# Kernel tuning notes

Measured on AMD Instinct MI355X. Metric: run time of the kernel, lower is better.

Reference implementation:

```python
import jax, jax.numpy as jnp
import numpy as np

TEMP = 0.5  # init temperature
EPS = 1e-12  # F.normalize eps


def setup_inputs() -> dict:
    key = jax.random.key(0)
    k1, k2 = jax.random.split(key)
    batch_embedding = jax.random.normal(k1, (4096, 256), dtype=jnp.float32)
    labels = jax.random.randint(k2, (4096,), 0, 512, dtype=jnp.int64)
    return {"batch_embedding": batch_embedding, "labels": labels}


def reference(batch_embedding, labels):
    n = labels.shape[0]
    dt = batch_embedding.dtype
    # row-normalize; cosine_similarity of normalized rows == norm @ norm.T
    nrm = jnp.linalg.norm(batch_embedding, axis=1, keepdims=True)
    norm = batch_embedding / jnp.maximum(nrm, EPS)
    sim = norm @ norm.T  # [n, n]
    mask = (labels[:, None] == labels[None, :]).astype(dt)  # same-label pairs (incl. diagonal)
    eye = jnp.eye(n, dtype=dt)
    exp_sim = jnp.exp(sim / TEMP) * (1.0 - eye)  # zero diagonal
    pos = mask * exp_sim
    neg_sum = jnp.sum(exp_sim - pos, axis=1)  # per-row negative sum
    ratio = pos / (pos + neg_sum[:, None])
    loss_mat = -jnp.log((1.0 - mask) + ratio + eye)
    nnz = jnp.count_nonzero(loss_mat).astype(dt)
    return jnp.sum(loss_mat) / nnz
```

## Files before the change

### kernel.cpp

```cpp
#include <hip/hip_runtime.h>
#include <hip/hip_bf16.h>


#define N_ROWS 4096
#define K_DIM  256

typedef __attribute__((ext_vector_type(8))) short short8;
typedef __attribute__((ext_vector_type(4))) float float4v;
typedef __attribute__((ext_vector_type(4))) float f4;

#define PK_OFF    0
#define PART_OFF  (N_ROWS * K_DIM * 2)
#define ACC_OFF   (PART_OFF + 4 * 64 * N_ROWS * 4)

__global__ void normalize_kernel(const float* __restrict__ emb,
                                 short* __restrict__ pk,
                                 float* __restrict__ acc) {
    int tile = blockIdx.x, t = threadIdx.x;
    __shared__ float lds[16 * 256];
    __shared__ float sc[16];
    const f4* src = (const f4*)(emb + tile * 16 * 256);
    f4* dst4 = (f4*)lds;
    #pragma unroll
    for (int it = 0; it < 4; ++it) dst4[t + 256 * it] = src[t + 256 * it];
    __syncthreads();
    int wave = t >> 6, lane = t & 63;
    int row = wave * 4 + (lane >> 4);
    float s = 0.f;
    #pragma unroll
    for (int m = 0; m < 16; ++m) {
        float x = lds[row * 256 + (lane & 15) + 16 * m];
        s += x * x;
    }
    s += __shfl_xor(s, 1); s += __shfl_xor(s, 2);
    s += __shfl_xor(s, 4); s += __shfl_xor(s, 8);
    float scale = 1.0f / fmaxf(sqrtf(s), 1e-12f);
    if ((lane & 15) == 0) sc[row] = scale;
    __syncthreads();
    short out[16];
    #pragma unroll
    for (int u = 0; u < 16; ++u) {
        int p = t * 16 + u;
        int j = p & 7, r16 = (p >> 3) & 15, quad = (p >> 7) & 3, c = p >> 9;
        int k = quad * 8 + c * 32 + j;
        float v = lds[r16 * 256 + k] * sc[r16];
        __hip_bfloat16 b = __float2bfloat16(v);
        out[u] = *(short*)&b;
    }
    short* dst = pk + tile * 4096 + t * 16;
    *(short8*)dst = *(short8*)out;
    *(short8*)(dst + 8) = *(short8*)(out + 8);
    if (tile == 0 && t < 2) acc[t] = 0.0f;
}

__global__ __launch_bounds__(256, 2)
void negsum_kernel(const short* __restrict__ pk,
                   const int* __restrict__ labels,
                   float* __restrict__ part) {
    int w = threadIdx.x >> 6, lane = threadIdx.x & 63;
    int lane16 = lane & 15, quad = lane >> 4;
    int wid = blockIdx.x * 4 + w;
    int i64 = wid >> 6, j64 = wid & 63;
    int ibase = i64 * 64, jbase = j64 * 64;

    int labi[16], labj[4];
    #pragma unroll
    for (int it = 0; it < 4; ++it)
        #pragma unroll
        for (int r = 0; r < 4; ++r)
            labi[it * 4 + r] = labels[ibase + it * 16 + quad * 4 + r];
    #pragma unroll
    for (int jt = 0; jt < 4; ++jt)
        labj[jt] = labels[jbase + jt * 16 + lane16];

    float4v acc[4][4];
    #pragma unroll
    for (int a = 0; a < 4; ++a)
        #pragma unroll
        for (int b = 0; b < 4; ++b)
            acc[a][b] = (float4v){0.f, 0.f, 0.f, 0.f};

    for (int c = 0; c < 8; ++c) {
        short8 af[4], bf[4];
        #pragma unroll
        for (int it = 0; it < 4; ++it)
            af[it] = *(const short8*)(pk + (((i64 * 4 + it) << 12) | (c << 9)) + lane * 8);
        #pragma unroll
        for (int jt = 0; jt < 4; ++jt)
            bf[jt] = *(const short8*)(pk + (((j64 * 4 + jt) << 12) | (c << 9)) + lane * 8);
        #pragma unroll
        for (int it = 0; it < 4; ++it)
            #pragma unroll
            for (int jt = 0; jt < 4; ++jt)
                acc[it][jt] = __builtin_amdgcn_mfma_f32_16x16x32_bf16(
                    af[it], bf[jt], acc[it][jt], 0, 0, 0);
    }

    float ex[4] = {0,0,0,0}, pe[4] = {0,0,0,0};
    float tt[4] = {0,0,0,0}, pc[4] = {0,0,0,0};
    #pragma unroll
    for (int it = 0; it < 4; ++it) {
        #pragma unroll
        for (int jt = 0; jt < 4; ++jt) {
            int j = jbase + jt * 16 + lane16;
            #pragma unroll
            for (int r = 0; r < 4; ++r) {
                int i = ibase + it * 16 + quad * 4 + r;
                float t2 = 2.0f * acc[it][jt][r];
                float e  = __expf(t2);
                bool keep = (i != j);
                bool same = (labi[it * 4 + r] == labj[jt]);
                ex[jt] += keep ? e : 0.0f;
                float m = (same && keep) ? 1.0f : 0.0f;
                pe[jt] = fmaf(m, e,  pe[jt]);
                tt[jt] = fmaf(m, t2, tt[jt]);
                pc[jt] += m;
            }
        }
    }

    #pragma unroll
    for (int jt = 0; jt < 4; ++jt) {
        float v0 = ex[jt], v1 = pe[jt], v2 = tt[jt], v3 = pc[jt];
        v0 += __shfl_xor(v0, 16); v0 += __shfl_xor(v0, 32);
        v1 += __shfl_xor(v1, 16); v1 += __shfl_xor(v1, 32);
        v2 += __shfl_xor(v2, 16); v2 += __shfl_xor(v2, 32);
        v3 += __shfl_xor(v3, 16); v3 += __shfl_xor(v3, 32);
        if (quad == 0) {
            int col = jbase + jt * 16 + lane16;
            part[((0 * 64 + i64) << 12) + col] = v0;
            part[((1 * 64 + i64) << 12) + col] = v1;
            part[((2 * 64 + i64) << 12) + col] = v2;
            part[((3 * 64 + i64) << 12) + col] = v3;
        }
    }
}

__global__ void rowreduce_kernel(const float* __restrict__ part,
                                 float* __restrict__ acc) {
    int j = blockIdx.x * 256 + threadIdx.x;
    float ex = 0.f, pe = 0.f, tt = 0.f, pc = 0.f;
    for (int ch = 0; ch < 64; ++ch) {
        ex += part[((0 * 64 + ch) << 12) + j];
        pe += part[((1 * 64 + ch) << 12) + j];
        tt += part[((2 * 64 + ch) << 12) + j];
        pc += part[((3 * 64 + ch) << 12) + j];
    }
    float lsum = 0.f;
    if (pc > 0.f) {
        float n = ex - pe;
        lsum = pc * logf(n) + pe / n - tt;
    } else {
        pc = 0.f;
    }
    #pragma unroll
    for (int off = 32; off > 0; off >>= 1) {
        lsum += __shfl_down(lsum, off, 64);
        pc   += __shfl_down(pc,   off, 64);
    }
    __shared__ float sl[4], sc2[4];
    int wave = threadIdx.x >> 6, lane = threadIdx.x & 63;
    if (lane == 0) { sl[wave] = lsum; sc2[wave] = pc; }
    __syncthreads();
    if (threadIdx.x == 0) {
        atomicAdd(&acc[0], sl[0] + sl[1] + sl[2] + sl[3]);
        atomicAdd(&acc[1], sc2[0] + sc2[1] + sc2[2] + sc2[3]);
    }
}

__global__ void div_kernel(const float* __restrict__ acc, float* __restrict__ out) {
    if (threadIdx.x == 0) out[0] = acc[0] / acc[1];
}

extern "C" void kernel_launch(void* const* d_in, const int* in_sizes, int n_in,
                              void* d_out, int out_size, void* d_ws, size_t ws_size,
                              hipStream_t stream) {
    const float* emb    = (const float*)d_in[0];
    const int*   labels = (const int*)d_in[1];
    float* out = (float*)d_out;
    char*  ws  = (char*)d_ws;

    short* pk   = (short*)(ws + PK_OFF);
    float* part = (float*)(ws + PART_OFF);
    float* acc  = (float*)(ws + ACC_OFF);

    normalize_kernel<<<N_ROWS / 16, 256, 0, stream>>>(emb, pk, acc);
    negsum_kernel<<<1024, 256, 0, stream>>>(pk, labels, part);
    rowreduce_kernel<<<16, 256, 0, stream>>>(part, acc);
    div_kernel<<<1, 64, 0, stream>>>(acc, out);
}
```

Before: 91.70 us.

## Share 128x128 block tiles via LDS and fold final divide into row reduce

New measurement: 89.47 us. -2.4%, faster.

```diff
diff --git a/kernel.cpp b/kernel.cpp
--- a/kernel.cpp
+++ b/kernel.cpp
@@ -12,6 +12,12 @@
 #define PK_OFF    0
 #define PART_OFF  (N_ROWS * K_DIM * 2)
 #define ACC_OFF   (PART_OFF + 4 * 64 * N_ROWS * 4)
+
+__device__ __forceinline__ void gll16(const void* g, void* l) {
+    __builtin_amdgcn_global_load_lds(
+        (const __attribute__((address_space(1))) unsigned int*)g,
+        (__attribute__((address_space(3))) unsigned int*)l, 16, 0, 0);
+}
 
 __global__ void normalize_kernel(const float* __restrict__ emb,
                                  short* __restrict__ pk,
@@ -50,19 +56,23 @@
     short* dst = pk + tile * 4096 + t * 16;
     *(short8*)dst = *(short8*)out;
     *(short8*)(dst + 8) = *(short8*)(out + 8);
-    if (tile == 0 && t < 2) acc[t] = 0.0f;
-}
-
-__global__ __launch_bounds__(256, 2)
+    if (tile == 0 && t < 4) acc[t] = 0.0f;
+}
+
+__global__ __launch_bounds__(256, 3)
 void negsum_kernel(const short* __restrict__ pk,
                    const int* __restrict__ labels,
                    float* __restrict__ part) {
-    int w = threadIdx.x >> 6, lane = threadIdx.x & 63;
+    __shared__ short As[8192];
+    __shared__ short Bs[8192];
+    int t = threadIdx.x;
+    int w = t >> 6, lane = t & 63;
     int lane16 = lane & 15, quad = lane >> 4;
-    int wid = blockIdx.x * 4 + w;
-    int i64 = wid >> 6, j64 = wid & 63;
-    int ibase = i64 * 64, jbase = j64 * 64;
-
+    int bi = blockIdx.x >> 5, bj = blockIdx.x & 31;
+    int wi = w >> 1, wj = w & 1;
+
+    int ibase = bi * 128 + wi * 64;
+    int jbase = bj * 128 + wj * 64;
     int labi[16], labj[4];
     #pragma unroll
     for (int it = 0; it < 4; ++it)
@@ -80,20 +90,44 @@
         for (int b = 0; b < 4; ++b)
             acc[a][b] = (float4v){0.f, 0.f, 0.f, 0.f};
 
-    for (int c = 0; c < 8; ++c) {
-        short8 af[4], bf[4];
-        #pragma unroll
-        for (int it = 0; it < 4; ++it)
-            af[it] = *(const short8*)(pk + (((i64 * 4 + it) << 12) | (c << 9)) + lane * 8);
-        #pragma unroll
-        for (int jt = 0; jt < 4; ++jt)
-            bf[jt] = *(const short8*)(pk + (((j64 * 4 + jt) << 12) | (c << 9)) + lane * 8);
-        #pragma unroll
-        for (int it = 0; it < 4; ++it)
+    const char* pkb = (const char*)pk;
+
+    for (int ks = 0; ks < 4; ++ks) {
+        if (ks) __syncthreads();
+        if (w < 2) {
+            #pragma unroll
+            for (int u = 0; u < 8; ++u) {
+                int a = w * 8 + u, tl = a >> 1, cs = a & 1;
+                gll16(pkb + (((bi * 8 + tl) << 13) | ((ks * 2 + cs) << 10)) + lane * 16,
+                      (char*)As + (a << 10));
+            }
+        } else {
+            #pragma unroll
+            for (int u = 0; u < 8; ++u) {
+                int a = (w - 2) * 8 + u, tl = a >> 1, cs = a & 1;
+                gll16(pkb + (((bj * 8 + tl) << 13) | ((ks * 2 + cs) << 10)) + lane * 16,
+                      (char*)Bs + (a << 10));
+            }
+        }
+        __syncthreads();
+        #pragma unroll
+        for (int cs = 0; cs < 2; ++cs) {
+            short8 af[4], bf[4];
+            #pragma unroll
+            for (int it = 0; it < 4; ++it)
+                af[it] = *(const short8*)((const char*)As
+                         + ((((wi * 4 + it) * 2 + cs) << 10)) + lane * 16);
             #pragma unroll
             for (int jt = 0; jt < 4; ++jt)
-                acc[it][jt] = __builtin_amdgcn_mfma_f32_16x16x32_bf16(
-                    af[it], bf[jt], acc[it][jt], 0, 0, 0);
+                bf[jt] = *(const short8*)((const char*)Bs
+                         + ((((wj * 4 + jt) * 2 + cs) << 10)) + lane * 16);
+            #pragma unroll
+            for (int it = 0; it < 4; ++it)
+                #pragma unroll
+                for (int jt = 0; jt < 4; ++jt)
+                    acc[it][jt] = __builtin_amdgcn_mfma_f32_16x16x32_bf16(
+                        af[it], bf[jt], acc[it][jt], 0, 0, 0);
+        }
     }
 
     float ex[4] = {0,0,0,0}, pe[4] = {0,0,0,0};
@@ -118,7 +152,7 @@
             }
         }
     }
-
+    int i64 = bi * 2 + wi;
     #pragma unroll
     for (int jt = 0; jt < 4; ++jt) {
         float v0 = ex[jt], v1 = pe[jt], v2 = tt[jt], v3 = pc[jt];
@@ -137,7 +171,8 @@
 }
 
 __global__ void rowreduce_kernel(const float* __restrict__ part,
-                                 float* __restrict__ acc) {
+                                 float* __restrict__ acc,
+                                 float* __restrict__ out) {
     int j = blockIdx.x * 256 + threadIdx.x;
     float ex = 0.f, pe = 0.f, tt = 0.f, pc = 0.f;
     for (int ch = 0; ch < 64; ++ch) {
@@ -165,11 +200,14 @@
     if (threadIdx.x == 0) {
         atomicAdd(&acc[0], sl[0] + sl[1] + sl[2] + sl[3]);
         atomicAdd(&acc[1], sc2[0] + sc2[1] + sc2[2] + sc2[3]);
-    }
-}
-
-__global__ void div_kernel(const float* __restrict__ acc, float* __restrict__ out) {
-    if (threadIdx.x == 0) out[0] = acc[0] / acc[1];
+        __threadfence();
+        int ticket = atomicAdd((int*)(acc + 2), 1);
+        if (ticket == 15) {
+            float ls = atomicAdd(&acc[0], 0.0f);
+            float cs = atomicAdd(&acc[1], 0.0f);
+            out[0] = ls / cs;
+        }
+    }
 }
 
 extern "C" void kernel_launch(void* const* d_in, const int* in_sizes, int n_in,
@@ -186,6 +224,5 @@
 
     normalize_kernel<<<N_ROWS / 16, 256, 0, stream>>>(emb, pk, acc);
     negsum_kernel<<<1024, 256, 0, stream>>>(pk, labels, part);
-    rowreduce_kernel<<<16, 256, 0, stream>>>(part, acc);
-    div_kernel<<<1, 64, 0, stream>>>(acc, out);
-}
+    rowreduce_kernel<<<16, 256, 0, stream>>>(part, acc, out);
+}
```
